# Kernel optimization log

Hardware: AMD Instinct MI355X
Metric: run time of the kernel (lower is better)

## Reference

```python
import jax, jax.numpy as jnp
import numpy as np

N = 100_000
E = 1_000_000
D = 64
NORM_FACTOR = 100.0
LN_EPS = 1e-5


def setup_inputs() -> dict:
    key = jax.random.key(0)
    ks = jax.random.split(key, 8)
    h = jax.random.normal(ks[0], (N, D), dtype=jnp.float32)
    distances = jax.random.uniform(ks[1], (E, 1), dtype=jnp.float32)
    edges = jax.random.randint(ks[2], (2, E), 0, N, dtype=jnp.int64)
    node_mask = jnp.ones((N, 1), dtype=jnp.float32)
    edge_mask = jnp.ones((E, 1), dtype=jnp.float32)
    s = 1.0 / np.sqrt(D)
    W_lin = jax.random.normal(ks[3], (D, D), dtype=jnp.float32) * s
    b_lin = jnp.zeros((D,), dtype=jnp.float32)
    att_W1 = jax.random.normal(ks[4], (D, 2 * D + 1), dtype=jnp.float32) * (1.0 / np.sqrt(2 * D + 1))
    att_b1 = jnp.zeros((D,), dtype=jnp.float32)
    att_W2 = jax.random.normal(ks[5], (1, D), dtype=jnp.float32) * s
    att_b2 = jnp.zeros((1,), dtype=jnp.float32)
    ln_g = jnp.ones((D,), dtype=jnp.float32)
    ln_b = jnp.zeros((D,), dtype=jnp.float32)
    return {"h": h, "distances": distances, "edges": edges, "node_mask": node_mask,
            "edge_mask": edge_mask, "W_lin": W_lin, "b_lin": b_lin,
            "att_W1": att_W1, "att_b1": att_b1, "att_W2": att_W2, "att_b2": att_b2,
            "ln_g": ln_g, "ln_b": ln_b}


def reference(h, distances, edges, node_mask, edge_mask, W_lin, b_lin,
              att_W1, att_b1, att_W2, att_b2, ln_g, ln_b):
    # Linear projection: [N, D]
    x = h @ W_lin.T + b_lin
    row, col = edges[0], edges[1]
    x_row = x[row]          # [E, D]
    x_col = x[col]          # [E, D]
    # DenseAtt: MLP(concat(x_row, x_col, dist)) -> sigmoid -> * edge_mask
    cat = jnp.concatenate([x_row, x_col, distances], axis=1)  # [E, 2D+1]
    hdn = jax.nn.silu(cat @ att_W1.T + att_b1)                # [E, D]
    att = jax.nn.sigmoid(hdn @ att_W2.T + att_b2) * edge_mask # [E, 1]
    # Attention-weighted scatter-sum aggregation into row segments
    agg = x_col * att
    out = jax.ops.segment_sum(agg, row, num_segments=x.shape[0]) / NORM_FACTOR
    out = out + x           # residual
    # LayerNorm + activation
    mu = jnp.mean(out, axis=-1, keepdims=True)
    var = jnp.mean(jnp.square(out - mu), axis=-1, keepdims=True)
    y = (out - mu) * jax.lax.rsqrt(var + LN_EPS) * ln_g + ln_b
    return jax.nn.silu(y)
```

## Files before the change

kernel.cpp:

```cpp
#include <hip/hip_runtime.h>
#include <hip/hip_bf16.h>

#define N_NODES 100000
#define N_EDGES 1000000
#define DIM 64
#define NORM_INV 0.01f
#define LN_EPS 1e-5f
#define N_TILES 6250
#define PROJ_BLOCKS 1563
#define N_BUCKETS 1563
#define HB_PK 784
#define SC_EDGES 4096
#define SC_BLOCKS 245
#define OFS_STRIDE 1568
#define L2E 1.4426950408889634f
#define LN2 0.6931471805599453f
#define CAP 1280

typedef __attribute__((ext_vector_type(8))) short short8;
typedef __attribute__((ext_vector_type(4))) float f32x4;

__device__ __forceinline__ unsigned short f2bf(float f) {
    union { float f; unsigned u; } x; x.f = f;
    unsigned r = x.u + 0x7FFFu + ((x.u >> 16) & 1u);
    return (unsigned short)(r >> 16);
}
__device__ __forceinline__ float bf2f(unsigned short s) {
    union { unsigned u; float f; } x; x.u = ((unsigned)s) << 16; return x.f;
}

__global__ __launch_bounds__(256) void proj_scatter(
    const float* __restrict__ h, const float* __restrict__ bl,
    const float* __restrict__ W, const float* __restrict__ att_W1,
    const int* __restrict__ edges, const float* __restrict__ dist,
    const float* __restrict__ emask,
    uint2* __restrict__ srec, unsigned short* __restrict__ ofsT,
    unsigned short* __restrict__ xv, unsigned short* __restrict__ u_bf) {
    __shared__ __align__(16) char pool[39168];
    __shared__ int wsum[4];

    if (blockIdx.x < SC_BLOCKS) {
        int* lh = (int*)pool;
        int* lofsP = (int*)pool + HB_PK;
        uint2* lsort = (uint2*)(pool + 6272);
        const int blk = blockIdx.x;
        const int tid = threadIdx.x;
        const int lane = tid & 63;
        const int w = tid >> 6;
        for (int i = tid; i < HB_PK; i += 256) lh[i] = 0;
        __syncthreads();

        const int eb = blk * SC_EDGES;
        const int total = min(SC_EDGES, N_EDGES - eb);

        int rows[16], rank[16];
        uint2 recs[16];
        const int e0 = eb + tid * 16;
#pragma unroll
        for (int g = 0; g < 4; ++g) {
            const int e = e0 + g * 4;
            if (e + 4 <= N_EDGES) {
                const int4 rr = *(const int4*)(edges + e);
                const int4 cc = *(const int4*)(edges + N_EDGES + e);
                const float4 dd = *(const float4*)(dist + e);
                const float4 mm = *(const float4*)(emask + e);
                rows[g*4+0] = rr.x; rows[g*4+1] = rr.y; rows[g*4+2] = rr.z; rows[g*4+3] = rr.w;
                const int c4[4] = {cc.x, cc.y, cc.z, cc.w};
                const float d4[4] = {dd.x, dd.y, dd.z, dd.w};
                const float m4[4] = {mm.x, mm.y, mm.z, mm.w};
#pragma unroll
                for (int i = 0; i < 4; ++i) {
                    const int ii = g * 4 + i;
                    recs[ii].x = (unsigned)c4[i] | ((unsigned)(rows[ii] & 63) << 24);
                    recs[ii].y = (unsigned)f2bf(d4[i]) |
                                 ((unsigned)f2bf(m4[i] * NORM_INV) << 16);
                    const int bk = rows[ii] >> 6;
                    const int sh = (bk & 1) << 4;
                    rank[ii] = (atomicAdd(&lh[bk >> 1], 1 << sh) >> sh) & 0xffff;
                }
            } else {
#pragma unroll
                for (int i = 0; i < 4; ++i) {
                    const int ii = g * 4 + i;
                    const int ee = e + i;
                    if (ee < N_EDGES) {
                        rows[ii] = edges[ee];
                        recs[ii].x = (unsigned)edges[N_EDGES + ee] |
                                     ((unsigned)(rows[ii] & 63) << 24);
                        recs[ii].y = (unsigned)f2bf(dist[ee]) |
                                     ((unsigned)f2bf(emask[ee] * NORM_INV) << 16);
                        const int bk = rows[ii] >> 6;
                        const int sh = (bk & 1) << 4;
                        rank[ii] = (atomicAdd(&lh[bk >> 1], 1 << sh) >> sh) & 0xffff;
                    } else {
                        rows[ii] = -1;
                    }
                }
            }
        }
        __syncthreads();

        const int t4 = tid * 4;
        int li[4];
#pragma unroll
        for (int g = 0; g < 4; ++g) li[g] = (t4 + g < HB_PK) ? lh[t4 + g] : 0;
        int cs[8];
#pragma unroll
        for (int g = 0; g < 4; ++g) {
            cs[2*g]   = li[g] & 0xffff;
            cs[2*g+1] = (li[g] >> 16) & 0xffff;
        }
        int S = 0;
#pragma unroll
        for (int k = 0; k < 8; ++k) S += cs[k];
        int sc = S;
#pragma unroll
        for (int off = 1; off < 64; off <<= 1) {
            int u = __shfl_up(sc, off);
            if (lane >= off) sc += u;
        }
        if (lane == 63) wsum[w] = sc;
        __syncthreads();
        int wbase = 0;
        if (w > 0) wbase = wsum[0];
        if (w > 1) wbase += wsum[1];
        if (w > 2) wbase += wsum[2];
        int run = sc - S + wbase;
#pragma unroll
        for (int g = 0; g < 4; ++g) {
            const int lo = run; run += cs[2*g];
            const int hi = run; run += cs[2*g+1];
            if (t4 + g < HB_PK) lofsP[t4 + g] = (unsigned)lo | ((unsigned)hi << 16);
        }
        __syncthreads();

#pragma unroll
        for (int i = 0; i < 16; ++i) {
            if (rows[i] >= 0) {
                const int bk = rows[i] >> 6;
                const int base = (lofsP[bk >> 1] >> ((bk & 1) << 4)) & 0xffff;
                lsort[base + rank[i]] = recs[i];
            }
        }
        __syncthreads();

        for (int s = tid; s < total; s += 256)
            srec[(size_t)blk * SC_EDGES + s] = lsort[s];
        for (int b = tid; b < 1564; b += 256)
            ofsT[blk * OFS_STRIDE + b] =
                (unsigned short)((lofsP[b >> 1] >> ((b & 1) << 4)) & 0xffff);
        return;
    }

    const int tid = threadIdx.x;
    const int lane = tid & 63;
    const int wv = tid >> 6;
    const int c = lane & 15, q = lane >> 4;

    {
        short8* Lwhi_w = (short8*)pool;
        short8* Lwlo_w = Lwhi_w + 512;
        short8* Lwa_w  = Lwhi_w + 1024;
        short8* Lwb_w  = Lwhi_w + 1536;
        const int nt_b = tid >> 6;
        const int n_b = nt_b * 16 + c;
#pragma unroll
        for (int ks = 0; ks < 2; ++ks) {
            const int k0 = ks * 32 + q * 8;
            short8 hi8, lo8, a8, b8;
#pragma unroll
            for (int jj = 0; jj < 8; ++jj) {
                float w = W[n_b * 64 + k0 + jj];
                unsigned short hh = f2bf(w);
                hi8[jj] = (short)hh;
                lo8[jj] = (short)f2bf(w - bf2f(hh));
                a8[jj] = (short)f2bf(att_W1[n_b * 129 + k0 + jj]);
                b8[jj] = (short)f2bf(att_W1[n_b * 129 + 64 + k0 + jj]);
            }
            const int idx = (nt_b * 2 + ks) * 64 + lane;
            Lwhi_w[idx] = hi8; Lwlo_w[idx] = lo8; Lwa_w[idx] = a8; Lwb_w[idx] = b8;
        }
    }
    __syncthreads();
    const short8* Lwhi = (const short8*)pool;
    const short8* Lwlo = Lwhi + 512;
    const short8* Lwa  = Lwhi + 1024;
    const short8* Lwb  = Lwhi + 1536;

    const int tile = (blockIdx.x - SC_BLOCKS) * 4 + wv;
    const bool valid = (tile < N_TILES);
    const int n0 = valid ? tile * 16 : 0;

    float bias[4];
#pragma unroll
    for (int nt = 0; nt < 4; ++nt) bias[nt] = bl[nt * 16 + c];

    short8 Ahi[2], Alo[2];
#pragma unroll
    for (int ks = 0; ks < 2; ++ks) {
        const float* hp = h + (size_t)(n0 + c) * 64 + ks * 32 + q * 8;
        f32x4 p0 = *(const f32x4*)hp;
        f32x4 p1 = *(const f32x4*)(hp + 4);
        short8 hi8, lo8;
#pragma unroll
        for (int jj = 0; jj < 4; ++jj) {
            unsigned short hh = f2bf(p0[jj]);
            hi8[jj] = (short)hh; lo8[jj] = (short)f2bf(p0[jj] - bf2f(hh));
            unsigned short h2 = f2bf(p1[jj]);
            hi8[4 + jj] = (short)h2; lo8[4 + jj] = (short)f2bf(p1[jj] - bf2f(h2));
        }
        Ahi[ks] = hi8; Alo[ks] = lo8;
    }

    f32x4 xacc[4] = {{0,0,0,0},{0,0,0,0},{0,0,0,0},{0,0,0,0}};
#pragma unroll
    for (int ks = 0; ks < 2; ++ks)
#pragma unroll
        for (int nt = 0; nt < 4; ++nt) {
            const short8 fhi = Lwhi[(nt * 2 + ks) * 64 + lane];
            const short8 flo = Lwlo[(nt * 2 + ks) * 64 + lane];
            xacc[nt] = __builtin_amdgcn_mfma_f32_16x16x32_bf16(Ahi[ks], fhi, xacc[nt], 0, 0, 0);
            xacc[nt] = __builtin_amdgcn_mfma_f32_16x16x32_bf16(Ahi[ks], flo, xacc[nt], 0, 0, 0);
            xacc[nt] = __builtin_amdgcn_mfma_f32_16x16x32_bf16(Alo[ks], fhi, xacc[nt], 0, 0, 0);
        }

    __syncthreads();

    unsigned short* lw = (unsigned short*)pool + wv * (16 * 72);
#pragma unroll
    for (int r = 0; r < 4; ++r) {
        const int node = n0 + q * 4 + r;
        unsigned short xb[4];
#pragma unroll
        for (int nt = 0; nt < 4; ++nt) {
            unsigned short v16 = f2bf(xacc[nt][r] + bias[nt]);
            xb[nt] = v16;
            lw[(q * 4 + r) * 72 + nt * 16 + c] = v16;
        }
        if (valid) {
            uint2 pk;
            pk.x = (unsigned)xb[0] | ((unsigned)xb[1] << 16);
            pk.y = (unsigned)xb[2] | ((unsigned)xb[3] << 16);
            *(uint2*)(xv + (size_t)node * 128 + c * 8) = pk;
        }
    }

    short8 Ax[2];
#pragma unroll
    for (int ks = 0; ks < 2; ++ks)
        Ax[ks] = *(const short8*)&lw[c * 72 + ks * 32 + q * 8];

    f32x4 uacc[4] = {{0,0,0,0},{0,0,0,0},{0,0,0,0},{0,0,0,0}};
    f32x4 vacc[4] = {{0,0,0,0},{0,0,0,0},{0,0,0,0},{0,0,0,0}};
#pragma unroll
    for (int ks = 0; ks < 2; ++ks)
#pragma unroll
        for (int nt = 0; nt < 4; ++nt) {
            const short8 fa = Lwa[(nt * 2 + ks) * 64 + lane];
            const short8 fb = Lwb[(nt * 2 + ks) * 64 + lane];
            uacc[nt] = __builtin_amdgcn_mfma_f32_16x16x32_bf16(Ax[ks], fa, uacc[nt], 0, 0, 0);
            vacc[nt] = __builtin_amdgcn_mfma_f32_16x16x32_bf16(Ax[ks], fb, vacc[nt], 0, 0, 0);
        }
    if (valid) {
#pragma unroll
        for (int r = 0; r < 4; ++r) {
            const int node = n0 + q * 4 + r;
            uint2 pu;
            pu.x = (unsigned)f2bf(uacc[0][r] * L2E) | ((unsigned)f2bf(uacc[1][r] * L2E) << 16);
            pu.y = (unsigned)f2bf(uacc[2][r] * L2E) | ((unsigned)f2bf(uacc[3][r] * L2E) << 16);
            *(uint2*)(u_bf + (size_t)node * 64 + c * 4) = pu;
            uint2 pk;
            pk.x = (unsigned)f2bf(vacc[0][r] * L2E) | ((unsigned)f2bf(vacc[1][r] * L2E) << 16);
            pk.y = (unsigned)f2bf(vacc[2][r] * L2E) | ((unsigned)f2bf(vacc[3][r] * L2E) << 16);
            *(uint2*)(xv + (size_t)node * 128 + c * 8 + 4) = pk;
        }
    }
}

__global__ __launch_bounds__(256, 8) void agg_fused(
    const uint2* __restrict__ srec, const unsigned short* __restrict__ ofsT,
    const unsigned short* __restrict__ xv, const unsigned short* __restrict__ u_bf,
    const float* __restrict__ att_W1, const float* __restrict__ att_b1,
    const float* __restrict__ att_W2, const float* __restrict__ att_b2,
    const float* __restrict__ ln_g, const float* __restrict__ ln_b,
    float* __restrict__ out) {
    __shared__ __align__(16) uint2 lrecs[CAP + 16];
    __shared__ float4 ltab[64];
    __shared__ int hist[64];
    __shared__ int rst[65];
    __shared__ int cur[64];
    __shared__ int sst[256];
    __shared__ int dbase[257];
    __shared__ int wsum4[4];

    const int b = blockIdx.x;
    const int tid = threadIdx.x;
    const int lane = tid & 63;
    const int wv = tid >> 6;

    if (tid < 64) hist[tid] = 0;
    if (tid >= 192) {
        const int f = tid - 192;
        ltab[f] = make_float4(att_W2[f] * LN2, att_W1[f * 129 + 128] * L2E,
                              att_b1[f] * L2E, 0.f);
    }

    int stv = 0, len = 0, sc0 = 0;
    {
        if (tid < SC_BLOCKS) {
            stv = (int)ofsT[tid * OFS_STRIDE + b];
            len = (int)ofsT[tid * OFS_STRIDE + b + 1] - stv;
        }
        sst[tid] = stv;
        sc0 = len;
#pragma unroll
        for (int off = 1; off < 64; off <<= 1) {
            int u = __shfl_up(sc0, off);
            if (lane >= off) sc0 += u;
        }
        if (lane == 63) wsum4[wv] = sc0;
    }
    __syncthreads();
    {
        int wbase = 0;
        if (wv > 0) wbase = wsum4[0];
        if (wv > 1) wbase += wsum4[1];
        if (wv > 2) wbase += wsum4[2];
        dbase[tid] = wbase + sc0 - len;
        if (tid == 255) dbase[256] = wbase + sc0;
    }
    __syncthreads();
    const int cnt = dbase[245];

    uint2 rec0, rec1, rec2, rec3;
    int lr0 = -1, lr1 = -1, lr2 = -1, lr3 = -1;
#define GATHER(I, RC, LR)                                                     \
    {                                                                         \
        const int m = tid + I * 256;                                          \
        if (m < cnt) {                                                        \
            int lo = 0, hi = 245;                                             \
            while (hi - lo > 1) {                                             \
                const int mid = (lo + hi) >> 1;                               \
                if (dbase[mid] <= m) lo = mid; else hi = mid;                 \
            }                                                                 \
            RC = srec[(size_t)lo * SC_EDGES + sst[lo] + (m - dbase[lo])];     \
            LR = (int)(RC.x >> 24);                                           \
            RC.x &= 0x00FFFFFFu;                                              \
            atomicAdd(&hist[LR], 1);                                          \
        }                                                                     \
    }
    GATHER(0, rec0, lr0)
    GATHER(1, rec1, lr1)
    GATHER(2, rec2, lr2)
    GATHER(3, rec3, lr3)
#undef GATHER
    __syncthreads();

    if (tid < 64) {
        const int c = hist[tid];
        const int p = (c + 3) & ~3;
        int sc = p;
#pragma unroll
        for (int off = 1; off < 64; off <<= 1) {
            int u = __shfl_up(sc, off);
            if (lane >= off) sc += u;
        }
        const int excl = sc - p;
        rst[tid] = excl;
        cur[tid] = excl;
        uint2 z; z.x = 0; z.y = 0;
        for (int i = c; i < p; ++i) lrecs[excl + i] = z;
        if (tid == 63) {
            rst[64] = excl + p;
            for (int i = 0; i < 16; ++i) lrecs[excl + p + i] = z;
        }
    }
    __syncthreads();

    if (lr0 >= 0) lrecs[atomicAdd(&cur[lr0], 1)] = rec0;
    if (lr1 >= 0) lrecs[atomicAdd(&cur[lr1], 1)] = rec1;
    if (lr2 >= 0) lrecs[atomicAdd(&cur[lr2], 1)] = rec2;
    if (lr3 >= 0) lrecs[atomicAdd(&cur[lr3], 1)] = rec3;
    __syncthreads();

    const int j = lane & 15;
    const int sl = lane >> 4;
    const float4 t0 = ltab[j], t1 = ltab[j + 16], t2 = ltab[j + 32], t3 = ltab[j + 48];
    const float b2L = att_b2[0] * L2E;
    const float gg = ln_g[lane], bb = ln_b[lane];
    const unsigned* xvu = (const unsigned*)xv;

#pragma unroll 1
    for (int k = 0; k < 16; ++k) {
        const int lrw = wv + 4 * k;
        const int r = b * 64 + lrw;
        if (r >= N_NODES) break;

        const uint2 uu = *(const uint2*)(u_bf + (size_t)r * 64 + j * 4);
        const float base0 = __uint_as_float(uu.x << 16) + t0.z;
        const float base1 = __uint_as_float(uu.x & 0xffff0000u) + t1.z;
        const float base2 = __uint_as_float(uu.y << 16) + t2.z;
        const float base3 = __uint_as_float(uu.y & 0xffff0000u) + t3.z;

        const int s0 = rst[lrw];
        const int e1 = rst[lrw + 1];

        float a0 = 0.f, a1 = 0.f, a2 = 0.f, a3 = 0.f;
        if (e1 > s0) {
            uint2 recA = lrecs[s0 + sl];
            uint2 recB = lrecs[s0 + 4 + sl];
            uint4 xvA = *(const uint4*)(xvu + (size_t)recA.x * 64 + j * 4);
            uint4 xvB = *(const uint4*)(xvu + (size_t)recB.x * 64 + j * 4);
            for (int e = s0; e < e1; e += 4) {
                const uint2 recC = lrecs[e + 8 + sl];
                const uint4 xvC = *(const uint4*)(xvu + (size_t)recC.x * 64 + j * 4);

                const float dist = __uint_as_float(recA.y << 16);
                const float emN = __uint_as_float(recA.y & 0xffff0000u);
                const float x0 = __uint_as_float(xvA.x << 16);
                const float x1 = __uint_as_float(xvA.x & 0xffff0000u);
                const float x2 = __uint_as_float(xvA.y << 16);
                const float x3 = __uint_as_float(xvA.y & 0xffff0000u);
                const float v0 = __uint_as_float(xvA.z << 16);
                const float v1 = __uint_as_float(xvA.z & 0xffff0000u);
                const float v2 = __uint_as_float(xvA.w << 16);
                const float v3 = __uint_as_float(xvA.w & 0xffff0000u);
                float pv = 0.f, pre, sg;
                pre = fmaf(dist, t0.y, base0) + v0;
                sg = __builtin_amdgcn_rcpf(1.f + __builtin_amdgcn_exp2f(-pre));
                pv = fmaf(pre * sg, t0.x, pv);
                pre = fmaf(dist, t1.y, base1) + v1;
                sg = __builtin_amdgcn_rcpf(1.f + __builtin_amdgcn_exp2f(-pre));
                pv = fmaf(pre * sg, t1.x, pv);
                pre = fmaf(dist, t2.y, base2) + v2;
                sg = __builtin_amdgcn_rcpf(1.f + __builtin_amdgcn_exp2f(-pre));
                pv = fmaf(pre * sg, t2.x, pv);
                pre = fmaf(dist, t3.y, base3) + v3;
                sg = __builtin_amdgcn_rcpf(1.f + __builtin_amdgcn_exp2f(-pre));
                pv = fmaf(pre * sg, t3.x, pv);
                pv += __shfl_xor(pv, 1); pv += __shfl_xor(pv, 2);
                pv += __shfl_xor(pv, 4); pv += __shfl_xor(pv, 8);
                const float sp = fmaf(pv, L2E, b2L);
                const float att =
                    emN * __builtin_amdgcn_rcpf(1.f + __builtin_amdgcn_exp2f(-sp));
                a0 = fmaf(att, x0, a0); a1 = fmaf(att, x1, a1);
                a2 = fmaf(att, x2, a2); a3 = fmaf(att, x3, a3);
                recA = recB; xvA = xvB; recB = recC; xvB = xvC;
            }
        }
        a0 += __shfl_xor(a0, 16); a0 += __shfl_xor(a0, 32);
        a1 += __shfl_xor(a1, 16); a1 += __shfl_xor(a1, 32);
        a2 += __shfl_xor(a2, 16); a2 += __shfl_xor(a2, 32);
        a3 += __shfl_xor(a3, 16); a3 += __shfl_xor(a3, 32);

        const uint2 xr = *(const uint2*)(xvu + (size_t)r * 64 + j * 4);
        const float o0 = __uint_as_float(xr.x << 16) + a0;
        const float o1 = __uint_as_float(xr.x & 0xffff0000u) + a1;
        const float o2 = __uint_as_float(xr.y << 16) + a2;
        const float o3 = __uint_as_float(xr.y & 0xffff0000u) + a3;

        float ssum = o0 + o1 + o2 + o3;
        ssum += __shfl_xor(ssum, 1); ssum += __shfl_xor(ssum, 2);
        ssum += __shfl_xor(ssum, 4); ssum += __shfl_xor(ssum, 8);
        const float mu = ssum * (1.f / 64.f);
        const float d0 = o0 - mu, d1 = o1 - mu, d2 = o2 - mu, d3 = o3 - mu;
        float vs = d0 * d0 + d1 * d1 + d2 * d2 + d3 * d3;
        vs += __shfl_xor(vs, 1); vs += __shfl_xor(vs, 2);
        vs += __shfl_xor(vs, 4); vs += __shfl_xor(vs, 8);
        const float rstd = rsqrtf(vs * (1.f / 64.f) + LN_EPS);

        const float dk = (sl == 0) ? d0 : (sl == 1) ? d1 : (sl == 2) ? d2 : d3;
        const float y = fmaf(dk * rstd, gg, bb);
        out[(size_t)r * 64 + lane] =
            y * __builtin_amdgcn_rcpf(1.f + __builtin_amdgcn_exp2f(-y * L2E));
    }
}

extern "C" void kernel_launch(void* const* d_in, const int* in_sizes, int n_in,
                              void* d_out, int out_size, void* d_ws, size_t ws_size,
                              hipStream_t stream) {
    const float* h      = (const float*)d_in[0];
    const float* dist   = (const float*)d_in[1];
    const int*   edges  = (const int*)d_in[2];
    const float* emask  = (const float*)d_in[4];
    const float* W_lin  = (const float*)d_in[5];
    const float* b_lin  = (const float*)d_in[6];
    const float* att_W1 = (const float*)d_in[7];
    const float* att_b1 = (const float*)d_in[8];
    const float* att_W2 = (const float*)d_in[9];
    const float* att_b2 = (const float*)d_in[10];
    const float* ln_g   = (const float*)d_in[11];
    const float* ln_b   = (const float*)d_in[12];
    float* out = (float*)d_out;

    char* ws = (char*)d_ws;
    unsigned short* xv   = (unsigned short*)ws;
    unsigned short* u_bf = (unsigned short*)(ws + 25600000);
    uint2* srec          = (uint2*)(ws + 38400000);
    unsigned short* ofsT = (unsigned short*)(ws + 46428160);

    proj_scatter<<<SC_BLOCKS + PROJ_BLOCKS, 256, 0, stream>>>(
        h, b_lin, W_lin, att_W1, edges, dist, emask, srec, ofsT, xv, u_bf);
    agg_fused<<<N_BUCKETS, 256, 0, stream>>>(srec, ofsT, xv, u_bf,
                                             att_W1, att_b1, att_W2, att_b2,
                                             ln_g, ln_b, out);
}
```

Baseline: 192.1 us.

## Split fused projection/scatter kernel into two launches and merge xv stores

The combined kernel that branched on block index between edge bucket-sorting and node projection is split into two separate kernels, each with its own smaller shared-memory footprint and register allocation. The projection's two 8-byte stores per node row into xv are combined into one 16-byte store by keeping the packed x values in registers until the v results are ready. The split is meant to stop one branch's LDS and register needs from limiting occupancy of the other, and to cut the number of store instructions. In exchange it adds a kernel launch and serializes the two phases on the stream, so they can no longer overlap.

```diff
diff --git a/kernel.cpp b/kernel.cpp
--- a/kernel.cpp
+++ b/kernel.cpp
@@ -29,128 +29,128 @@
     union { unsigned u; float f; } x; x.u = ((unsigned)s) << 16; return x.f;
 }
 
-__global__ __launch_bounds__(256) void proj_scatter(
-    const float* __restrict__ h, const float* __restrict__ bl,
-    const float* __restrict__ W, const float* __restrict__ att_W1,
+__global__ __launch_bounds__(256) void scatter_k(
     const int* __restrict__ edges, const float* __restrict__ dist,
     const float* __restrict__ emask,
-    uint2* __restrict__ srec, unsigned short* __restrict__ ofsT,
-    unsigned short* __restrict__ xv, unsigned short* __restrict__ u_bf) {
-    __shared__ __align__(16) char pool[39168];
+    uint2* __restrict__ srec, unsigned short* __restrict__ ofsT) {
+    __shared__ __align__(16) char pool[39040];
     __shared__ int wsum[4];
-
-    if (blockIdx.x < SC_BLOCKS) {
-        int* lh = (int*)pool;
-        int* lofsP = (int*)pool + HB_PK;
-        uint2* lsort = (uint2*)(pool + 6272);
-        const int blk = blockIdx.x;
-        const int tid = threadIdx.x;
-        const int lane = tid & 63;
-        const int w = tid >> 6;
-        for (int i = tid; i < HB_PK; i += 256) lh[i] = 0;
-        __syncthreads();
-
-        const int eb = blk * SC_EDGES;
-        const int total = min(SC_EDGES, N_EDGES - eb);
-
-        int rows[16], rank[16];
-        uint2 recs[16];
-        const int e0 = eb + tid * 16;
-#pragma unroll
-        for (int g = 0; g < 4; ++g) {
-            const int e = e0 + g * 4;
-            if (e + 4 <= N_EDGES) {
-                const int4 rr = *(const int4*)(edges + e);
-                const int4 cc = *(const int4*)(edges + N_EDGES + e);
-                const float4 dd = *(const float4*)(dist + e);
-                const float4 mm = *(const float4*)(emask + e);
-                rows[g*4+0] = rr.x; rows[g*4+1] = rr.y; rows[g*4+2] = rr.z; rows[g*4+3] = rr.w;
-                const int c4[4] = {cc.x, cc.y, cc.z, cc.w};
-                const float d4[4] = {dd.x, dd.y, dd.z, dd.w};
-                const float m4[4] = {mm.x, mm.y, mm.z, mm.w};
-#pragma unroll
-                for (int i = 0; i < 4; ++i) {
-                    const int ii = g * 4 + i;
-                    recs[ii].x = (unsigned)c4[i] | ((unsigned)(rows[ii] & 63) << 24);
-                    recs[ii].y = (unsigned)f2bf(d4[i]) |
-                                 ((unsigned)f2bf(m4[i] * NORM_INV) << 16);
+    int* lh = (int*)pool;
+    int* lofsP = (int*)pool + HB_PK;
+    uint2* lsort = (uint2*)(pool + 6272);
+    const int blk = blockIdx.x;
+    const int tid = threadIdx.x;
+    const int lane = tid & 63;
+    const int w = tid >> 6;
+    for (int i = tid; i < HB_PK; i += 256) lh[i] = 0;
+    __syncthreads();
+
+    const int eb = blk * SC_EDGES;
+    const int total = min(SC_EDGES, N_EDGES - eb);
+
+    int rows[16], rank[16];
+    uint2 recs[16];
+    const int e0 = eb + tid * 16;
+#pragma unroll
+    for (int g = 0; g < 4; ++g) {
+        const int e = e0 + g * 4;
+        if (e + 4 <= N_EDGES) {
+            const int4 rr = *(const int4*)(edges + e);
+            const int4 cc = *(const int4*)(edges + N_EDGES + e);
+            const float4 dd = *(const float4*)(dist + e);
+            const float4 mm = *(const float4*)(emask + e);
+            rows[g*4+0] = rr.x; rows[g*4+1] = rr.y; rows[g*4+2] = rr.z; rows[g*4+3] = rr.w;
+            const int c4[4] = {cc.x, cc.y, cc.z, cc.w};
+            const float d4[4] = {dd.x, dd.y, dd.z, dd.w};
+            const float m4[4] = {mm.x, mm.y, mm.z, mm.w};
+#pragma unroll
+            for (int i = 0; i < 4; ++i) {
+                const int ii = g * 4 + i;
+                recs[ii].x = (unsigned)c4[i] | ((unsigned)(rows[ii] & 63) << 24);
+                recs[ii].y = (unsigned)f2bf(d4[i]) |
+                             ((unsigned)f2bf(m4[i] * NORM_INV) << 16);
+                const int bk = rows[ii] >> 6;
+                const int sh = (bk & 1) << 4;
+                rank[ii] = (atomicAdd(&lh[bk >> 1], 1 << sh) >> sh) & 0xffff;
+            }
+        } else {
+#pragma unroll
+            for (int i = 0; i < 4; ++i) {
+                const int ii = g * 4 + i;
+                const int ee = e + i;
+                if (ee < N_EDGES) {
+                    rows[ii] = edges[ee];
+                    recs[ii].x = (unsigned)edges[N_EDGES + ee] |
+                                 ((unsigned)(rows[ii] & 63) << 24);
+                    recs[ii].y = (unsigned)f2bf(dist[ee]) |
+                                 ((unsigned)f2bf(emask[ee] * NORM_INV) << 16);
                     const int bk = rows[ii] >> 6;
                     const int sh = (bk & 1) << 4;
                     rank[ii] = (atomicAdd(&lh[bk >> 1], 1 << sh) >> sh) & 0xffff;
-                }
-            } else {
-#pragma unroll
-                for (int i = 0; i < 4; ++i) {
-                    const int ii = g * 4 + i;
-                    const int ee = e + i;
-                    if (ee < N_EDGES) {
-                        rows[ii] = edges[ee];
-                        recs[ii].x = (unsigned)edges[N_EDGES + ee] |
-                                     ((unsigned)(rows[ii] & 63) << 24);
-                        recs[ii].y = (unsigned)f2bf(dist[ee]) |
-                                     ((unsigned)f2bf(emask[ee] * NORM_INV) << 16);
-                        const int bk = rows[ii] >> 6;
-                        const int sh = (bk & 1) << 4;
-                        rank[ii] = (atomicAdd(&lh[bk >> 1], 1 << sh) >> sh) & 0xffff;
-                    } else {
-                        rows[ii] = -1;
-                    }
+                } else {
+                    rows[ii] = -1;
                 }
             }
         }
-        __syncthreads();
-
-        const int t4 = tid * 4;
-        int li[4];
-#pragma unroll
-        for (int g = 0; g < 4; ++g) li[g] = (t4 + g < HB_PK) ? lh[t4 + g] : 0;
-        int cs[8];
-#pragma unroll
-        for (int g = 0; g < 4; ++g) {
-            cs[2*g]   = li[g] & 0xffff;
-            cs[2*g+1] = (li[g] >> 16) & 0xffff;
-        }
-        int S = 0;
-#pragma unroll
-        for (int k = 0; k < 8; ++k) S += cs[k];
-        int sc = S;
-#pragma unroll
-        for (int off = 1; off < 64; off <<= 1) {
-            int u = __shfl_up(sc, off);
-            if (lane >= off) sc += u;
-        }
-        if (lane == 63) wsum[w] = sc;
-        __syncthreads();
-        int wbase = 0;
-        if (w > 0) wbase = wsum[0];
-        if (w > 1) wbase += wsum[1];
-        if (w > 2) wbase += wsum[2];
-        int run = sc - S + wbase;
-#pragma unroll
-        for (int g = 0; g < 4; ++g) {
-            const int lo = run; run += cs[2*g];
-            const int hi = run; run += cs[2*g+1];
-            if (t4 + g < HB_PK) lofsP[t4 + g] = (unsigned)lo | ((unsigned)hi << 16);
-        }
-        __syncthreads();
-
-#pragma unroll
-        for (int i = 0; i < 16; ++i) {
-            if (rows[i] >= 0) {
-                const int bk = rows[i] >> 6;
-                const int base = (lofsP[bk >> 1] >> ((bk & 1) << 4)) & 0xffff;
-                lsort[base + rank[i]] = recs[i];
-            }
-        }
-        __syncthreads();
-
-        for (int s = tid; s < total; s += 256)
-            srec[(size_t)blk * SC_EDGES + s] = lsort[s];
-        for (int b = tid; b < 1564; b += 256)
-            ofsT[blk * OFS_STRIDE + b] =
-                (unsigned short)((lofsP[b >> 1] >> ((b & 1) << 4)) & 0xffff);
-        return;
-    }
+    }
+    __syncthreads();
+
+    const int t4 = tid * 4;
+    int li[4];
+#pragma unroll
+    for (int g = 0; g < 4; ++g) li[g] = (t4 + g < HB_PK) ? lh[t4 + g] : 0;
+    int cs[8];
+#pragma unroll
+    for (int g = 0; g < 4; ++g) {
+        cs[2*g]   = li[g] & 0xffff;
+        cs[2*g+1] = (li[g] >> 16) & 0xffff;
+    }
+    int S = 0;
+#pragma unroll
+    for (int k = 0; k < 8; ++k) S += cs[k];
+    int sc = S;
+#pragma unroll
+    for (int off = 1; off < 64; off <<= 1) {
+        int u = __shfl_up(sc, off);
+        if (lane >= off) sc += u;
+    }
+    if (lane == 63) wsum[w] = sc;
+    __syncthreads();
+    int wbase = 0;
+    if (w > 0) wbase = wsum[0];
+    if (w > 1) wbase += wsum[1];
+    if (w > 2) wbase += wsum[2];
+    int run = sc - S + wbase;
+#pragma unroll
+    for (int g = 0; g < 4; ++g) {
+        const int lo = run; run += cs[2*g];
+        const int hi = run; run += cs[2*g+1];
+        if (t4 + g < HB_PK) lofsP[t4 + g] = (unsigned)lo | ((unsigned)hi << 16);
+    }
+    __syncthreads();
+
+#pragma unroll
+    for (int i = 0; i < 16; ++i) {
+        if (rows[i] >= 0) {
+            const int bk = rows[i] >> 6;
+            const int base = (lofsP[bk >> 1] >> ((bk & 1) << 4)) & 0xffff;
+            lsort[base + rank[i]] = recs[i];
+        }
+    }
+    __syncthreads();
+
+    for (int s = tid; s < total; s += 256)
+        srec[(size_t)blk * SC_EDGES + s] = lsort[s];
+    for (int b = tid; b < 1564; b += 256)
+        ofsT[blk * OFS_STRIDE + b] =
+            (unsigned short)((lofsP[b >> 1] >> ((b & 1) << 4)) & 0xffff);
+}
+
+__global__ __launch_bounds__(256) void proj_k(
+    const float* __restrict__ h, const float* __restrict__ bl,
+    const float* __restrict__ W, const float* __restrict__ att_W1,
+    unsigned short* __restrict__ xv, unsigned short* __restrict__ u_bf) {
+    __shared__ __align__(16) char pool[32768];
 
     const int tid = threadIdx.x;
     const int lane = tid & 63;
@@ -187,7 +187,7 @@
     const short8* Lwa  = Lwhi + 1024;
     const short8* Lwb  = Lwhi + 1536;
 
-    const int tile = (blockIdx.x - SC_BLOCKS) * 4 + wv;
+    const int tile = blockIdx.x * 4 + wv;
     const bool valid = (tile < N_TILES);
     const int n0 = valid ? tile * 16 : 0;
 
@@ -227,9 +227,9 @@
     __syncthreads();
 
     unsigned short* lw = (unsigned short*)pool + wv * (16 * 72);
+    uint2 xpk[4];
 #pragma unroll
     for (int r = 0; r < 4; ++r) {
-        const int node = n0 + q * 4 + r;
         unsigned short xb[4];
 #pragma unroll
         for (int nt = 0; nt < 4; ++nt) {
@@ -237,12 +237,8 @@
             xb[nt] = v16;
             lw[(q * 4 + r) * 72 + nt * 16 + c] = v16;
         }
-        if (valid) {
-            uint2 pk;
-            pk.x = (unsigned)xb[0] | ((unsigned)xb[1] << 16);
-            pk.y = (unsigned)xb[2] | ((unsigned)xb[3] << 16);
-            *(uint2*)(xv + (size_t)node * 128 + c * 8) = pk;
-        }
+        xpk[r].x = (unsigned)xb[0] | ((unsigned)xb[1] << 16);
+        xpk[r].y = (unsigned)xb[2] | ((unsigned)xb[3] << 16);
     }
 
     short8 Ax[2];
@@ -269,10 +265,12 @@
             pu.x = (unsigned)f2bf(uacc[0][r] * L2E) | ((unsigned)f2bf(uacc[1][r] * L2E) << 16);
             pu.y = (unsigned)f2bf(uacc[2][r] * L2E) | ((unsigned)f2bf(uacc[3][r] * L2E) << 16);
             *(uint2*)(u_bf + (size_t)node * 64 + c * 4) = pu;
-            uint2 pk;
-            pk.x = (unsigned)f2bf(vacc[0][r] * L2E) | ((unsigned)f2bf(vacc[1][r] * L2E) << 16);
-            pk.y = (unsigned)f2bf(vacc[2][r] * L2E) | ((unsigned)f2bf(vacc[3][r] * L2E) << 16);
-            *(uint2*)(xv + (size_t)node * 128 + c * 8 + 4) = pk;
+            uint4 pk;
+            pk.x = xpk[r].x;
+            pk.y = xpk[r].y;
+            pk.z = (unsigned)f2bf(vacc[0][r] * L2E) | ((unsigned)f2bf(vacc[1][r] * L2E) << 16);
+            pk.w = (unsigned)f2bf(vacc[2][r] * L2E) | ((unsigned)f2bf(vacc[3][r] * L2E) << 16);
+            *(uint4*)(xv + (size_t)node * 128 + c * 8) = pk;
         }
     }
 }
@@ -499,8 +497,8 @@
     uint2* srec          = (uint2*)(ws + 38400000);
     unsigned short* ofsT = (unsigned short*)(ws + 46428160);
 
-    proj_scatter<<<SC_BLOCKS + PROJ_BLOCKS, 256, 0, stream>>>(
-        h, b_lin, W_lin, att_W1, edges, dist, emask, srec, ofsT, xv, u_bf);
+    scatter_k<<<SC_BLOCKS, 256, 0, stream>>>(edges, dist, emask, srec, ofsT);
+    proj_k<<<PROJ_BLOCKS, 256, 0, stream>>>(h, b_lin, W_lin, att_W1, xv, u_bf);
     agg_fused<<<N_BUCKETS, 256, 0, stream>>>(srec, ofsT, xv, u_bf,
                                              att_W1, att_b1, att_W2, att_b2,
                                              ln_g, ln_b, out);
```

New measurement: 197.2 us. +2.7%, slower.
